# Kernel optimization log

Measured on AMD Instinct MI355X. Metric: run time of the kernel, lower is better.

Reference implementation:

```python
import jax, jax.numpy as jnp
import numpy as np

N_USERS = 50000
N_ITEMS = 100000
N_NODES = N_USERS + N_ITEMS
N_EDGES = 2400000
D = 64
N_LAYERS = 3


def setup_inputs() -> dict:
    key = jax.random.key(0)
    ks = jax.random.split(key, 9)
    edge_src = jax.random.randint(ks[0], (N_EDGES,), 0, N_NODES, dtype=jnp.int32)
    edge_dst = jax.random.randint(ks[1], (N_EDGES,), 0, N_NODES, dtype=jnp.int32)
    edge_vals = jax.random.uniform(ks[2], (N_EDGES,), dtype=jnp.float32)
    user_emb = jax.random.normal(ks[3], (N_USERS, D), dtype=jnp.float32) * 0.1
    item_emb = jax.random.normal(ks[4], (N_ITEMS, D), dtype=jnp.float32) * 0.1
    Wgc = jax.random.normal(ks[5], (N_LAYERS, D, D), dtype=jnp.float32) * (1.0 / np.sqrt(D))
    bgc = jax.random.normal(ks[6], (N_LAYERS, D), dtype=jnp.float32) * 0.01
    Wbi = jax.random.normal(ks[7], (N_LAYERS, D, D), dtype=jnp.float32) * (1.0 / np.sqrt(D))
    bbi = jax.random.normal(ks[8], (N_LAYERS, D), dtype=jnp.float32) * 0.01
    return {"edge_src": edge_src, "edge_dst": edge_dst, "edge_vals": edge_vals,
            "user_emb": user_emb, "item_emb": item_emb,
            "Wgc": Wgc, "bgc": bgc, "Wbi": Wbi, "bbi": bbi}


def _spmm(edge_src, edge_dst, edge_vals, x, n_nodes):
    # adj @ x with adj in COO: out[d] = sum_e vals[e] * x[src[e]] for dst[e]==d
    msgs = edge_vals[:, None] * x[edge_src]          # [E, D]
    return jax.ops.segment_sum(msgs, edge_dst, num_segments=n_nodes)


def _l2norm(x, eps=1e-12):
    n = jnp.sqrt(jnp.sum(x * x, axis=1, keepdims=True))
    return x / jnp.maximum(n, eps)


def reference(edge_src, edge_dst, edge_vals, user_emb, item_emb, Wgc, bgc, Wbi, bbi):
    n_users = user_emb.shape[0]
    n_nodes = n_users + item_emb.shape[0]
    ego = jnp.concatenate([user_emb, item_emb], axis=0)  # [N, D]
    all_embs = [ego]
    for i in range(Wgc.shape[0]):
        side = _spmm(edge_src, edge_dst, edge_vals, ego, n_nodes)       # adj @ ego
        sum_e = jax.nn.leaky_relu(side @ Wgc[i].T + bgc[i])             # GC branch
        bi_e = jax.nn.leaky_relu((ego * side) @ Wbi[i].T + bbi[i])      # Bi branch
        ego = sum_e + bi_e                                              # dropout p=0 -> identity
        all_embs.append(_l2norm(ego))
    all_embs = jnp.concatenate(all_embs, axis=1)  # [N, D*(L+1)]
    return all_embs[:n_users], all_embs[n_users:]
```

## Files before the change

### kernel.cpp

```cpp
#include <hip/hip_runtime.h>

#define NU 50000
#define NI 100000
#define NN 150000
#define NE 2400000
#define DD 64
#define NL 3
#define CHUNK 1024
#define NB ((NN + CHUNK - 1) / CHUNK)

__global__ void init_kernel(const float* __restrict__ uemb, const float* __restrict__ iemb,
                            float* __restrict__ ego, float* __restrict__ out) {
    int i = blockIdx.x * blockDim.x + threadIdx.x;
    if (i >= NN * DD) return;
    int n = i >> 6, d = i & 63;
    float v = (n < NU) ? uemb[i] : iemb[i - NU * DD];
    ego[i] = v;
    out[n * (DD * (NL + 1)) + d] = v;
}

__global__ void hist_kernel(const int* __restrict__ dst, int* __restrict__ counts) {
    int e = blockIdx.x * blockDim.x + threadIdx.x;
    if (e < NE) atomicAdd(&counts[dst[e]], 1);
}

__global__ void scanA_kernel(const int* __restrict__ counts, int* __restrict__ bsum) {
    __shared__ int sh[256];
    int t = threadIdx.x, b = blockIdx.x;
    int base = b * CHUNK + t * 4;
    int s = 0;
#pragma unroll
    for (int i = 0; i < 4; ++i) { int idx = base + i; if (idx < NN) s += counts[idx]; }
    sh[t] = s; __syncthreads();
    for (int off = 128; off > 0; off >>= 1) {
        if (t < off) sh[t] += sh[t + off];
        __syncthreads();
    }
    if (t == 0) bsum[b] = sh[0];
}

__global__ void scanB_kernel(int* __restrict__ bsum, int* __restrict__ offs) {
    __shared__ int sh[256];
    int t = threadIdx.x;
    int v = (t < NB) ? bsum[t] : 0;
    sh[t] = v; __syncthreads();
    for (int off = 1; off < 256; off <<= 1) {
        int add = (t >= off) ? sh[t - off] : 0;
        __syncthreads();
        sh[t] += add;
        __syncthreads();
    }
    if (t < NB) bsum[t] = sh[t] - v;
    if (t == NB - 1) offs[NN] = sh[t];
}

__global__ void scanC_kernel(const int* __restrict__ counts, const int* __restrict__ bsum,
                             int* __restrict__ offs) {
    __shared__ int sh[256];
    int t = threadIdx.x, b = blockIdx.x;
    int base = b * CHUNK + t * 4;
    int c[4]; int tsum = 0;
#pragma unroll
    for (int i = 0; i < 4; ++i) { int idx = base + i; c[i] = (idx < NN) ? counts[idx] : 0; tsum += c[i]; }
    sh[t] = tsum; __syncthreads();
    for (int off = 1; off < 256; off <<= 1) {
        int add = (t >= off) ? sh[t - off] : 0;
        __syncthreads();
        sh[t] += add;
        __syncthreads();
    }
    int excl = sh[t] - tsum + bsum[b];
#pragma unroll
    for (int i = 0; i < 4; ++i) {
        int idx = base + i;
        if (idx < NN) offs[idx] = excl;
        excl += c[i];
    }
}

__global__ void fill_kernel(const int* __restrict__ src, const int* __restrict__ dst,
                            const float* __restrict__ vals, const int* __restrict__ offs,
                            int* __restrict__ cursor, int2* __restrict__ pair) {
    int e = blockIdx.x * blockDim.x + threadIdx.x;
    if (e >= NE) return;
    int d = dst[e];
    int pos = offs[d] + atomicAdd(&cursor[d], 1);
    pair[pos] = make_int2(src[e], __float_as_int(vals[e]));
}

__global__ __launch_bounds__(256) void spmm_kernel(
        const int* __restrict__ offs, const int2* __restrict__ pair,
        const float* __restrict__ ego, float* __restrict__ side) {
    int gid = blockIdx.x * blockDim.x + threadIdx.x;
    int node = gid >> 6;
    if (node >= NN) return;
    int lane = threadIdx.x & 63;
    int sub = lane >> 4;
    int dq  = lane & 15;
    int beg = offs[node], end = offs[node + 1];
    float4 acc = make_float4(0.f, 0.f, 0.f, 0.f);
    int i = beg;
    for (; i + 4 <= end; i += 4) {
        int2 p = pair[i + sub];
        float w = __int_as_float(p.y);
        float4 v = ((const float4*)(ego + (size_t)p.x * DD))[dq];
        acc.x = fmaf(w, v.x, acc.x);
        acc.y = fmaf(w, v.y, acc.y);
        acc.z = fmaf(w, v.z, acc.z);
        acc.w = fmaf(w, v.w, acc.w);
    }
    if (i < end) {
        int r = end - i;
        if (sub < r) {
            int2 p = pair[i + sub];
            float w = __int_as_float(p.y);
            float4 v = ((const float4*)(ego + (size_t)p.x * DD))[dq];
            acc.x = fmaf(w, v.x, acc.x);
            acc.y = fmaf(w, v.y, acc.y);
            acc.z = fmaf(w, v.z, acc.z);
            acc.w = fmaf(w, v.w, acc.w);
        }
    }
    acc.x += __shfl_xor(acc.x, 16); acc.y += __shfl_xor(acc.y, 16);
    acc.z += __shfl_xor(acc.z, 16); acc.w += __shfl_xor(acc.w, 16);
    acc.x += __shfl_xor(acc.x, 32); acc.y += __shfl_xor(acc.y, 32);
    acc.z += __shfl_xor(acc.z, 32); acc.w += __shfl_xor(acc.w, 32);
    if (sub == 0) ((float4*)(side + (size_t)node * DD))[dq] = acc;
}

#define WPAD 65
#define UPD_TPB 256
#define UPD_GRID 1024
#define NPAIR (NN / 2)

__device__ __forceinline__ float rdlane(float v, int l) {
    return __int_as_float(__builtin_amdgcn_readlane(__float_as_int(v), l));
}

__global__ __launch_bounds__(UPD_TPB, 4) void update_kernel(
        const float* __restrict__ side, float* __restrict__ ego,
        const float* __restrict__ Wg, const float* __restrict__ bg,
        const float* __restrict__ Wb, const float* __restrict__ bb,
        float* __restrict__ out, int layer) {
    __shared__ float2 WT[64 * WPAD];
    int tid = threadIdx.x;
    int lane = tid & 63;

    for (int idx = tid; idx < 64 * 64; idx += UPD_TPB) {
        int j = idx >> 6, k = idx & 63;
        WT[k * WPAD + j] = make_float2(Wg[idx], Wb[idx]);
    }
    __syncthreads();

    float bgj = bg[lane], bbj = bb[lane];
    int nwaves = UPD_GRID * (UPD_TPB / 64);
    int gwave = blockIdx.x * (UPD_TPB / 64) + (tid >> 6);

    for (int g = gwave; g < NPAIR; g += nwaves) {
        int n0 = g * 2;
        float sv0 = side[(size_t)n0 * DD + lane];
        float sv1 = side[(size_t)(n0 + 1) * DD + lane];
        float mv0 = ego[(size_t)n0 * DD + lane] * sv0;
        float mv1 = ego[(size_t)(n0 + 1) * DD + lane] * sv1;
        float ag0 = bgj, ab0 = bbj, ag1 = bgj, ab1 = bbj;
#pragma unroll 4
        for (int k = 0; k < 64; ++k) {
            float2 w = WT[k * WPAD + lane];
            float sk0 = rdlane(sv0, k);
            float mk0 = rdlane(mv0, k);
            float sk1 = rdlane(sv1, k);
            float mk1 = rdlane(mv1, k);
            ag0 = fmaf(sk0, w.x, ag0);
            ab0 = fmaf(mk0, w.y, ab0);
            ag1 = fmaf(sk1, w.x, ag1);
            ab1 = fmaf(mk1, w.y, ab1);
        }
        ag0 = (ag0 > 0.f) ? ag0 : 0.01f * ag0;
        ab0 = (ab0 > 0.f) ? ab0 : 0.01f * ab0;
        ag1 = (ag1 > 0.f) ? ag1 : 0.01f * ag1;
        ab1 = (ab1 > 0.f) ? ab1 : 0.01f * ab1;
        float v0 = ag0 + ab0, v1 = ag1 + ab1;
        float sq0 = v0 * v0, sq1 = v1 * v1;
#pragma unroll
        for (int off = 1; off < 64; off <<= 1) {
            sq0 += __shfl_xor(sq0, off);
            sq1 += __shfl_xor(sq1, off);
        }
        float r0 = 1.f / fmaxf(sqrtf(sq0), 1e-12f);
        float r1 = 1.f / fmaxf(sqrtf(sq1), 1e-12f);
        ego[(size_t)n0 * DD + lane] = v0;
        ego[(size_t)(n0 + 1) * DD + lane] = v1;
        out[(size_t)n0 * (DD * (NL + 1)) + (layer + 1) * DD + lane] = v0 * r0;
        out[(size_t)(n0 + 1) * (DD * (NL + 1)) + (layer + 1) * DD + lane] = v1 * r1;
    }
}

extern "C" void kernel_launch(void* const* d_in, const int* in_sizes, int n_in,
                              void* d_out, int out_size, void* d_ws, size_t ws_size,
                              hipStream_t stream) {
    const int*   edge_src  = (const int*)d_in[0];
    const int*   edge_dst  = (const int*)d_in[1];
    const float* edge_vals = (const float*)d_in[2];
    const float* uemb      = (const float*)d_in[3];
    const float* iemb      = (const float*)d_in[4];
    const float* Wgc       = (const float*)d_in[5];
    const float* bgc       = (const float*)d_in[6];
    const float* Wbi       = (const float*)d_in[7];
    const float* bbi       = (const float*)d_in[8];
    float* out = (float*)d_out;

    char* p = (char*)d_ws;
    auto alloc = [&](size_t bytes) { char* r = p; p += (bytes + 255) & ~(size_t)255; return r; };
    int*   counts = (int*)alloc((size_t)NN * 4);
    int*   offs   = (int*)alloc((size_t)(NN + 1) * 4);
    int*   bsum   = (int*)alloc((size_t)NB * 4);
    int2*  pair   = (int2*)alloc((size_t)NE * 8);
    float* ego    = (float*)alloc((size_t)NN * DD * 4);
    float* side   = (float*)alloc((size_t)NN * DD * 4);

    hipMemsetAsync(counts, 0, (size_t)NN * 4, stream);
    init_kernel<<<(NN * DD + 255) / 256, 256, 0, stream>>>(uemb, iemb, ego, out);
    hist_kernel<<<(NE + 255) / 256, 256, 0, stream>>>(edge_dst, counts);
    scanA_kernel<<<NB, 256, 0, stream>>>(counts, bsum);
    scanB_kernel<<<1, 256, 0, stream>>>(bsum, offs);
    scanC_kernel<<<NB, 256, 0, stream>>>(counts, bsum, offs);
    hipMemsetAsync(counts, 0, (size_t)NN * 4, stream);
    fill_kernel<<<(NE + 255) / 256, 256, 0, stream>>>(edge_src, edge_dst, edge_vals, offs, counts, pair);

    for (int l = 0; l < NL; ++l) {
        spmm_kernel<<<(NN * 64 + 255) / 256, 256, 0, stream>>>(offs, pair, ego, side);
        update_kernel<<<UPD_GRID, UPD_TPB, 0, stream>>>(
            side, ego, Wgc + l * DD * DD, bgc + l * DD, Wbi + l * DD * DD, bbi + l * DD,
            out, l);
    }
}
```

Before: 1.065 ms.

## Hold weights in registers, broadcast activations via LDS, prefetch next node pair

The update kernel now keeps each lane's row of Wgc and Wbi in registers as 64 packed float2 values instead of reading a transposed weight copy from shared memory. Per-node activations (side and ego*side) go to a small per-wave LDS buffer and are read back as broadcasts, replacing the readlane calls, and the inner product uses packed two-wide FMAs. Loads for the next node pair are issued before the current pair's math so memory latency can overlap compute. The cost is a much higher register count, with launch bounds lowered from 4 to 3 waves per SIMD, which may reduce occupancy or cause spills.

```diff
diff --git a/kernel.cpp b/kernel.cpp
--- a/kernel.cpp
+++ b/kernel.cpp
@@ -128,53 +128,67 @@
     if (sub == 0) ((float4*)(side + (size_t)node * DD))[dq] = acc;
 }
 
-#define WPAD 65
+typedef float v2f __attribute__((ext_vector_type(2)));
 #define UPD_TPB 256
 #define UPD_GRID 1024
 #define NPAIR (NN / 2)
 
-__device__ __forceinline__ float rdlane(float v, int l) {
-    return __int_as_float(__builtin_amdgcn_readlane(__float_as_int(v), l));
-}
-
-__global__ __launch_bounds__(UPD_TPB, 4) void update_kernel(
+__global__ __launch_bounds__(UPD_TPB, 3) void update_kernel(
         const float* __restrict__ side, float* __restrict__ ego,
         const float* __restrict__ Wg, const float* __restrict__ bg,
         const float* __restrict__ Wb, const float* __restrict__ bb,
         float* __restrict__ out, int layer) {
-    __shared__ float2 WT[64 * WPAD];
+    __shared__ v2f sm[UPD_TPB / 64][2][DD];
     int tid = threadIdx.x;
     int lane = tid & 63;
-
-    for (int idx = tid; idx < 64 * 64; idx += UPD_TPB) {
-        int j = idx >> 6, k = idx & 63;
-        WT[k * WPAD + j] = make_float2(Wg[idx], Wb[idx]);
-    }
-    __syncthreads();
-
-    float bgj = bg[lane], bbj = bb[lane];
-    int nwaves = UPD_GRID * (UPD_TPB / 64);
-    int gwave = blockIdx.x * (UPD_TPB / 64) + (tid >> 6);
-
-    for (int g = gwave; g < NPAIR; g += nwaves) {
-        int n0 = g * 2;
-        float sv0 = side[(size_t)n0 * DD + lane];
-        float sv1 = side[(size_t)(n0 + 1) * DD + lane];
-        float mv0 = ego[(size_t)n0 * DD + lane] * sv0;
-        float mv1 = ego[(size_t)(n0 + 1) * DD + lane] * sv1;
-        float ag0 = bgj, ab0 = bbj, ag1 = bgj, ab1 = bbj;
-#pragma unroll 4
-        for (int k = 0; k < 64; ++k) {
-            float2 w = WT[k * WPAD + lane];
-            float sk0 = rdlane(sv0, k);
-            float mk0 = rdlane(mv0, k);
-            float sk1 = rdlane(sv1, k);
-            float mk1 = rdlane(mv1, k);
-            ag0 = fmaf(sk0, w.x, ag0);
-            ab0 = fmaf(mk0, w.y, ab0);
-            ag1 = fmaf(sk1, w.x, ag1);
-            ab1 = fmaf(mk1, w.y, ab1);
-        }
+    int wid = tid >> 6;
+
+    v2f w[DD];
+    {
+        const float4* g4 = (const float4*)(Wg + lane * DD);
+        const float4* b4 = (const float4*)(Wb + lane * DD);
+#pragma unroll
+        for (int k4 = 0; k4 < 16; ++k4) {
+            float4 a = g4[k4], b = b4[k4];
+            w[4 * k4 + 0] = (v2f){a.x, b.x};
+            w[4 * k4 + 1] = (v2f){a.y, b.y};
+            w[4 * k4 + 2] = (v2f){a.z, b.z};
+            w[4 * k4 + 3] = (v2f){a.w, b.w};
+        }
+    }
+    v2f bias = {bg[lane], bb[lane]};
+
+    const int nwaves = UPD_GRID * (UPD_TPB / 64);
+    int g = blockIdx.x * (UPD_TPB / 64) + wid;
+    if (g >= NPAIR) return;
+
+    float s0 = side[(size_t)(2 * g) * DD + lane];
+    float s1 = side[(size_t)(2 * g + 1) * DD + lane];
+    float e0 = ego[(size_t)(2 * g) * DD + lane];
+    float e1 = ego[(size_t)(2 * g + 1) * DD + lane];
+
+    while (true) {
+        sm[wid][0][lane] = (v2f){s0, s0 * e0};
+        sm[wid][1][lane] = (v2f){s1, s1 * e1};
+
+        int gn = g + nwaves;
+        bool more = gn < NPAIR;
+        int gl = more ? gn : g;
+        s0 = side[(size_t)(2 * gl) * DD + lane];
+        s1 = side[(size_t)(2 * gl + 1) * DD + lane];
+        e0 = ego[(size_t)(2 * gl) * DD + lane];
+        e1 = ego[(size_t)(2 * gl + 1) * DD + lane];
+
+        v2f acc0 = bias, acc1 = bias;
+#pragma unroll
+        for (int k = 0; k < DD; ++k) {
+            v2f a = sm[wid][0][k];
+            v2f b = sm[wid][1][k];
+            acc0 = __builtin_elementwise_fma(a, w[k], acc0);
+            acc1 = __builtin_elementwise_fma(b, w[k], acc1);
+        }
+
+        float ag0 = acc0.x, ab0 = acc0.y, ag1 = acc1.x, ab1 = acc1.y;
         ag0 = (ag0 > 0.f) ? ag0 : 0.01f * ag0;
         ab0 = (ab0 > 0.f) ? ab0 : 0.01f * ab0;
         ag1 = (ag1 > 0.f) ? ag1 : 0.01f * ag1;
@@ -188,10 +202,14 @@
         }
         float r0 = 1.f / fmaxf(sqrtf(sq0), 1e-12f);
         float r1 = 1.f / fmaxf(sqrtf(sq1), 1e-12f);
+        int n0 = 2 * g;
         ego[(size_t)n0 * DD + lane] = v0;
         ego[(size_t)(n0 + 1) * DD + lane] = v1;
         out[(size_t)n0 * (DD * (NL + 1)) + (layer + 1) * DD + lane] = v0 * r0;
         out[(size_t)(n0 + 1) * (DD * (NL + 1)) + (layer + 1) * DD + lane] = v1 * r1;
+
+        if (!more) break;
+        g = gn;
     }
 }
 
```

New measurement: 944.6 us. -11.3%, faster.
